# Kernel optimization log

Hardware: AMD Instinct MI355X
Metric: run time of the kernel (lower is better)

The kernel has to match this reference:

```python
import jax, jax.numpy as jnp
import numpy as np

NH = 16      # num_attention_heads
NKV = 8      # num_key_value_heads
G = NH // NKV  # num_key_value_groups
D = 128      # head_dim = hidden_size // NH
ROPE_MAX = 2048


def _rope_tables(seq_len, dtype=jnp.float32):
    # matches RotaryEmbedding: inv_freq over even dims, freqs duplicated (concat), cos/sin cached
    inv_freq = 1.0 / (10000.0 ** (jnp.arange(0, D, 2, dtype=jnp.float32) / D))
    t = jnp.arange(ROPE_MAX, dtype=jnp.float32)[:, None]          # [max, 1]
    freqs = t * inv_freq[None, :]                                  # [max, D/2]
    freqs = jnp.concatenate((freqs, freqs), axis=-1)               # [max, D]
    cos = jnp.cos(freqs)[:seq_len].astype(dtype)                   # [S, D]
    sin = jnp.sin(freqs)[:seq_len].astype(dtype)
    # unsqueeze(0) then unsqueeze(2) -> [1, S, 1, D] broadcasting over batch and heads
    return cos[None, :, None, :], sin[None, :, None, :]


def _rotate_half(x):
    x1, x2 = jnp.split(x, 2, axis=-1)
    return jnp.concatenate((-x2, x1), axis=-1)


def setup_inputs() -> dict:
    key = jax.random.key(0)
    ks = jax.random.split(key, 5)
    B, S, H = 2, 2048, 2048
    scale = 1.0 / np.sqrt(H)
    return {
        "hidden_states": jax.random.normal(ks[0], (B, S, H), jnp.float32),
        "Wq": jax.random.normal(ks[1], (H, H), jnp.float32) * scale,
        "Wk": jax.random.normal(ks[2], (NKV * D, H), jnp.float32) * scale,
        "Wv": jax.random.normal(ks[3], (NKV * D, H), jnp.float32) * scale,
        "Wo": jax.random.normal(ks[4], (H, H), jnp.float32) * scale,
    }


def reference(hidden_states, Wq, Wk, Wv, Wo):
    B, S, H = hidden_states.shape
    # projections (nn.Linear: y = x @ W.T, no bias)
    q = (hidden_states @ Wq.T).reshape(B, S, NH, D)     # [B,S,NH,D]
    k = (hidden_states @ Wk.T).reshape(B, S, NKV, D)    # [B,S,NKV,D]
    v = (hidden_states @ Wv.T).reshape(B, S, NKV, D)

    cos, sin = _rope_tables(S, hidden_states.dtype)
    q = q * cos + _rotate_half(q) * sin
    k = k * cos + _rotate_half(k) * sin

    # GQA: query head h attends to kv head h // G (repeat_kv ordering: h = n*G + g)
    qg = q.reshape(B, S, NKV, G, D).transpose(0, 2, 3, 1, 4)   # [B,NKV,G,S,D]
    kt = k.transpose(0, 2, 1, 3)                                # [B,NKV,S,D]
    vt = v.transpose(0, 2, 1, 3)                                # [B,NKV,S,D]

    scores = jnp.einsum("bngqd,bnkd->bngqk", qg, kt) / np.sqrt(D)  # [B,NKV,G,S,S]
    causal = jnp.triu(jnp.ones((S, S), dtype=bool), k=1)
    neg = jnp.finfo(scores.dtype).min
    scores = jnp.where(causal[None, None, None], neg, scores)
    probs = jax.nn.softmax(scores.astype(jnp.float32), axis=-1).astype(q.dtype)

    out = jnp.einsum("bngqk,bnkd->bngqd", probs, vt)            # [B,NKV,G,S,D]
    out = out.transpose(0, 3, 1, 2, 4).reshape(B, S, H)         # [B,S,H]
    return out @ Wo.T
```

## Files before the change

kernel.cpp:

```cpp
#include <hip/hip_runtime.h>

typedef unsigned short u16;
typedef __attribute__((ext_vector_type(8))) short short8;
typedef __attribute__((ext_vector_type(4))) float f32x4;

__device__ __forceinline__ u16 f2bf(float f) {
  unsigned u = __float_as_uint(f);
  return (u16)((u + 0x7FFFu + ((u >> 16) & 1u)) >> 16);
}
__device__ __forceinline__ float bf2f(u16 h) {
  return __uint_as_float(((unsigned)h) << 16);
}

__device__ __forceinline__ void gload_lds16(const void* g, void* l) {
  __builtin_amdgcn_global_load_lds(
      (const __attribute__((address_space(1))) unsigned*)g,
      (__attribute__((address_space(3))) unsigned*)l, 16, 0, 0);
}

__global__ void cast_f32_bf16_k(const float4* __restrict__ in, u16* __restrict__ out, int n4) {
  int i = blockIdx.x * 256 + threadIdx.x;
  if (i >= n4) return;
  float4 v = in[i];
  union { u16 u[4]; uint2 d; } r;
  r.u[0] = f2bf(v.x); r.u[1] = f2bf(v.y); r.u[2] = f2bf(v.z); r.u[3] = f2bf(v.w);
  *reinterpret_cast<uint2*>(out + (size_t)i * 4) = r.d;
}

__global__ void rope_tables_k(float* __restrict__ cosT, float* __restrict__ sinT) {
  int idx = blockIdx.x * 256 + threadIdx.x;
  int i = idx & 63, s = idx >> 6;
  double inv = pow(10000.0, -(double)(2 * i) / 128.0);
  double f = (double)s * inv;
  cosT[idx] = (float)cos(f);
  sinT[idx] = (float)sin(f);
}

__global__ void rope_q_k(u16* __restrict__ x, const float* __restrict__ cosT,
                         const float* __restrict__ sinT) {
  int idx = blockIdx.x * 256 + threadIdx.x;
  int i = idx & 63;
  int hh = (idx >> 6) & 15;
  int row = idx >> 10;
  int s = row & 2047;
  size_t base = (size_t)row * 4096 + hh * 128;
  float x1 = bf2f(x[base + i]);
  float x2 = bf2f(x[base + i + 64]);
  float c = cosT[s * 64 + i], sn = sinT[s * 64 + i];
  x[base + i]      = f2bf(x1 * c - x2 * sn);
  x[base + i + 64] = f2bf(x2 * c + x1 * sn);
}

__global__ void rope_repack_k_k(const u16* __restrict__ qkv, u16* __restrict__ kt,
                                const float* __restrict__ cosT, const float* __restrict__ sinT) {
  int idx = blockIdx.x * 256 + threadIdx.x;
  int i = idx & 63;
  int kvh = (idx >> 6) & 7;
  int row = idx >> 9;
  int s = row & 2047, b = row >> 11;
  size_t src = (size_t)row * 4096 + 2048 + kvh * 128;
  float x1 = bf2f(qkv[src + i]);
  float x2 = bf2f(qkv[src + i + 64]);
  float c = cosT[s * 64 + i], sn = sinT[s * 64 + i];
  size_t dst = ((size_t)(b * 8 + kvh) * 2048 + s) * 128;
  kt[dst + i]      = f2bf(x1 * c - x2 * sn);
  kt[dst + i + 64] = f2bf(x2 * c + x1 * sn);
}

__global__ void transpose_v_k(const u16* __restrict__ qkv, u16* __restrict__ vt) {
  __shared__ u16 tile[128][129];
  int bn = blockIdx.y;
  int s0 = blockIdx.x * 128;
  int b = bn >> 3, n = bn & 7;
  for (int e = threadIdx.x; e < 128 * 128; e += 256) {
    int r = e >> 7, c = e & 127;
    tile[r][c] = qkv[(size_t)(b * 2048 + s0 + r) * 4096 + 3072 + n * 128 + c];
  }
  __syncthreads();
  for (int e = threadIdx.x; e < 128 * 128; e += 256) {
    int r = e >> 7, c = e & 127;
    vt[((size_t)bn * 128 + r) * 2048 + s0 + c] = tile[c][r];
  }
}

template<typename OutT>
__global__ __launch_bounds__(256) void gemm_bt_k(
    const u16* __restrict__ A, const u16* __restrict__ Bm,
    OutT* __restrict__ C, int M, int N, int K)
{
  __shared__ __align__(16) u16 As[128 * 32];
  __shared__ __align__(16) u16 Bs[128 * 32];
  const int tid = threadIdx.x;
  const int wave = tid >> 6, lane = tid & 63;
  const int wr = wave >> 1, wc = wave & 1;
  const int lrow = lane & 15, lgrp = lane >> 4;
  const int nwg = (int)(gridDim.x * gridDim.y);
  const int f = (int)(blockIdx.y * gridDim.x + blockIdx.x);
  const int sw = (f & 7) * (nwg >> 3) + (f >> 3);
  const int bx = sw % gridDim.x, by = sw / gridDim.x;
  const int row0 = by * 128, col0 = bx * 128;

  f32x4 acc[4][4];
  #pragma unroll
  for (int m = 0; m < 4; ++m)
    #pragma unroll
    for (int n = 0; n < 4; ++n) acc[m][n] = (f32x4){0.f, 0.f, 0.f, 0.f};

  for (int k0 = 0; k0 < K; k0 += 32) {
    #pragma unroll
    for (int i = 0; i < 2; ++i) {
      int c = i * 256 + tid;
      int r = c >> 2, cc = ((c & 3) ^ (r & 3)) * 8;
      gload_lds16(A + (size_t)(row0 + r) * K + k0 + cc,
                  As + (size_t)(i * 256 + wave * 64) * 8);
      gload_lds16(Bm + (size_t)(col0 + r) * K + k0 + cc,
                  Bs + (size_t)(i * 256 + wave * 64) * 8);
    }
    __syncthreads();
    short8 af[4], bfr[4];
    #pragma unroll
    for (int m = 0; m < 4; ++m)
      af[m] = *reinterpret_cast<const short8*>(As + (wr * 64 + m * 16 + lrow) * 32 + (lgrp ^ (lrow & 3)) * 8);
    #pragma unroll
    for (int n = 0; n < 4; ++n)
      bfr[n] = *reinterpret_cast<const short8*>(Bs + (wc * 64 + n * 16 + lrow) * 32 + (lgrp ^ (lrow & 3)) * 8);
    #pragma unroll
    for (int m = 0; m < 4; ++m)
      #pragma unroll
      for (int n = 0; n < 4; ++n)
        acc[m][n] = __builtin_amdgcn_mfma_f32_16x16x32_bf16(af[m], bfr[n], acc[m][n], 0, 0, 0);
    __syncthreads();
  }
  #pragma unroll
  for (int m = 0; m < 4; ++m)
    #pragma unroll
    for (int n = 0; n < 4; ++n)
      #pragma unroll
      for (int j = 0; j < 4; ++j) {
        int r = row0 + wr * 64 + m * 16 + lgrp * 4 + j;
        int col = col0 + wc * 64 + n * 16 + lrow;
        float val = acc[m][n][j];
        if constexpr (sizeof(OutT) == 2) C[(size_t)r * N + col] = f2bf(val);
        else                             C[(size_t)r * N + col] = val;
      }
}

template<typename OutT>
__global__ __launch_bounds__(512, 1) void gemm256_k(
    const u16* __restrict__ A, const u16* __restrict__ Bm,
    OutT* __restrict__ C, int M, int N, int K)
{
  __shared__ __align__(16) u16 As[2][256 * 64];
  __shared__ __align__(16) u16 Bs[2][256 * 64];
  const int tid = threadIdx.x;
  const int wave = tid >> 6, lane = tid & 63;
  const int wm = wave >> 2, wn = wave & 3;
  const int lrow = lane & 15, lgrp = lane >> 4;
  const int gx = (int)gridDim.x;
  const int nwg = gx * (int)gridDim.y;
  const int f = (int)(blockIdx.y * gridDim.x + blockIdx.x);
  const int sw = (f & 7) * (nwg >> 3) + (f >> 3);
  const int bx = sw % gx, by = sw / gx;
  const int row0 = by * 256, col0 = bx * 256;

  f32x4 acc[8][4];
  #pragma unroll
  for (int m = 0; m < 8; ++m)
    #pragma unroll
    for (int n = 0; n < 4; ++n) acc[m][n] = (f32x4){0.f, 0.f, 0.f, 0.f};

  const int NT = K >> 6;

  auto stage = [&](int buf, int k0) {
    #pragma unroll
    for (int i = 0; i < 4; ++i) {
      int cid = i * 512 + tid;
      int row = cid >> 3, cp = cid & 7;
      int c = cp ^ (row & 7);
      gload_lds16(A + (size_t)(row0 + row) * K + k0 + c * 8,
                  &As[buf][(size_t)(i * 512 + wave * 64) * 8]);
      gload_lds16(Bm + (size_t)(col0 + row) * K + k0 + c * 8,
                  &Bs[buf][(size_t)(i * 512 + wave * 64) * 8]);
    }
  };

  stage(0, 0);
  for (int t = 0; t < NT; ++t) {
    const int cur = t & 1;
    if (t + 1 < NT) {
      stage(cur ^ 1, (t + 1) << 6);
      asm volatile("s_waitcnt vmcnt(8)" ::: "memory");
    } else {
      asm volatile("s_waitcnt vmcnt(0)" ::: "memory");
    }
    __builtin_amdgcn_s_barrier();
    __builtin_amdgcn_sched_barrier(0);
    #pragma unroll
    for (int ks = 0; ks < 2; ++ks) {
      short8 af[8], bfr[4];
      #pragma unroll
      for (int m = 0; m < 8; ++m) {
        int row = wm * 128 + m * 16 + lrow;
        int cp = (ks * 4 + lgrp) ^ (row & 7);
        af[m] = *reinterpret_cast<const short8*>(&As[cur][row * 64 + cp * 8]);
      }
      #pragma unroll
      for (int n = 0; n < 4; ++n) {
        int row = wn * 64 + n * 16 + lrow;
        int cp = (ks * 4 + lgrp) ^ (row & 7);
        bfr[n] = *reinterpret_cast<const short8*>(&Bs[cur][row * 64 + cp * 8]);
      }
      #pragma unroll
      for (int m = 0; m < 8; ++m)
        #pragma unroll
        for (int n = 0; n < 4; ++n)
          acc[m][n] = __builtin_amdgcn_mfma_f32_16x16x32_bf16(af[m], bfr[n], acc[m][n], 0, 0, 0);
    }
    __builtin_amdgcn_sched_barrier(0);
    __builtin_amdgcn_s_barrier();
  }

  #pragma unroll
  for (int m = 0; m < 8; ++m)
    #pragma unroll
    for (int n = 0; n < 4; ++n)
      #pragma unroll
      for (int j = 0; j < 4; ++j) {
        int r = row0 + wm * 128 + m * 16 + lgrp * 4 + j;
        int col = col0 + wn * 64 + n * 16 + lrow;
        float val = acc[m][n][j];
        if constexpr (sizeof(OutT) == 2) C[(size_t)r * N + col] = f2bf(val);
        else                             C[(size_t)r * N + col] = val;
      }
}

__global__ __launch_bounds__(256, 2) void flash_attn_k(
    const u16* __restrict__ qkv, const u16* __restrict__ kt,
    const u16* __restrict__ vt, u16* __restrict__ o)
{
  constexpr int S = 2048, NH = 16, NKV = 8, D = 128;
  const int wave = threadIdx.x >> 6, lane = threadIdx.x & 63;
  const int flat = blockIdx.x;
  const int pr = flat >> 5;
  const int bh = (flat & 7) * 4 + ((flat >> 3) & 3);
  const int b = bh >> 4, h = bh & 15;
  const int kvh = h >> 1;
  const int lrow = lane & 15, lgrp = lane >> 4;

  __shared__ __align__(16) u16 ks[2][64 * 128];
  __shared__ __align__(16) u16 vs[2][128 * 64];

  const float scl2 = 0.12754245006443634f;
  const u16* khead = kt + (size_t)(b * NKV + kvh) * S * D;
  const u16* vhead = vt + (size_t)(b * NKV + kvh) * D * S;

  auto stage = [&](int nxt, int kv0n) {
    #pragma unroll
    for (int i = 0; i < 4; ++i) {
      int c = i * 256 + wave * 64 + lane;
      int kr = c >> 4;
      int kc16 = (c & 15) ^ (kr & 7);
      gload_lds16(khead + (size_t)(kv0n + kr) * D + kc16 * 8,
                  &ks[nxt][(size_t)(i * 256 + wave * 64) * 8]);
      int vr = c >> 3;
      int vc = (c & 7) ^ (vr & 7);
      gload_lds16(vhead + (size_t)vr * S + kv0n + vc * 8,
                  &vs[nxt][(size_t)(i * 256 + wave * 64) * 8]);
    }
  };

  #pragma unroll
  for (int ph = 0; ph < 2; ++ph) {
    const int qt = ph ? pr : (31 - pr);
    const int q0 = qt * 64 + wave * 16;
    const int trips = qt + 1;

    short8 qf[4];
    const u16* qbase = qkv + (size_t)(b * S + q0 + lrow) * 4096 + h * 128;
    #pragma unroll
    for (int kc = 0; kc < 4; ++kc)
      qf[kc] = *reinterpret_cast<const short8*>(qbase + kc * 32 + lgrp * 8);

    f32x4 acc[8];
    #pragma unroll
    for (int n = 0; n < 8; ++n) acc[n] = (f32x4){0.f, 0.f, 0.f, 0.f};
    float l_part[4] = {0.f, 0.f, 0.f, 0.f};

    stage(0, 0);
    __syncthreads();

    for (int t = 0; t < trips; ++t) {
      const int cur = t & 1;
      const int kv0 = t * 64;
      f32x4 sc[4];
      #pragma unroll
      for (int nb = 0; nb < 4; ++nb) {
        sc[nb] = (f32x4){0.f, 0.f, 0.f, 0.f};
        const int r = nb * 16 + lrow;
        #pragma unroll
        for (int kc = 0; kc < 4; ++kc) {
          int ch = (kc * 4 + lgrp) ^ (r & 7);
          short8 kf = *reinterpret_cast<const short8*>(&ks[cur][r * 128 + ch * 8]);
          sc[nb] = __builtin_amdgcn_mfma_f32_16x16x32_bf16(qf[kc], kf, sc[nb], 0, 0, 0);
        }
      }
      __syncthreads();
      if (t + 1 < trips) stage(cur ^ 1, kv0 + 64);
      u16* pb = &ks[cur][wave * 1024];
      if (t < trips - 1) {
        #pragma unroll
        for (int nb = 0; nb < 4; ++nb)
          #pragma unroll
          for (int j = 0; j < 4; ++j) {
            int qr = lgrp * 4 + j;
            float p = exp2f(fminf(sc[nb][j] * scl2, 43.f));
            l_part[j] += p;
            pb[qr * 64 + ((nb * 16 + lrow) ^ ((qr & 7) << 3))] = f2bf(p);
          }
      } else {
        #pragma unroll
        for (int nb = 0; nb < 4; ++nb) {
          if (nb < wave) {
            #pragma unroll
            for (int j = 0; j < 4; ++j) {
              int qr = lgrp * 4 + j;
              float p = exp2f(fminf(sc[nb][j] * scl2, 43.f));
              l_part[j] += p;
              pb[qr * 64 + ((nb * 16 + lrow) ^ ((qr & 7) << 3))] = f2bf(p);
            }
          } else if (nb == wave) {
            #pragma unroll
            for (int j = 0; j < 4; ++j) {
              int qr = lgrp * 4 + j;
              float p = (lrow <= qr) ? exp2f(fminf(sc[nb][j] * scl2, 43.f)) : 0.f;
              l_part[j] += p;
              pb[qr * 64 + ((nb * 16 + lrow) ^ ((qr & 7) << 3))] = f2bf(p);
            }
          } else {
            #pragma unroll
            for (int j = 0; j < 4; ++j) {
              int qr = lgrp * 4 + j;
              pb[qr * 64 + ((nb * 16 + lrow) ^ ((qr & 7) << 3))] = 0;
            }
          }
        }
      }
      short8 pf[2];
      #pragma unroll
      for (int kc2 = 0; kc2 < 2; ++kc2) {
        int ch = (kc2 * 4 + lgrp) ^ (lrow & 7);
        pf[kc2] = *reinterpret_cast<const short8*>(&pb[lrow * 64 + ch * 8]);
      }
      #pragma unroll
      for (int n = 0; n < 8; ++n) {
        const int d = n * 16 + lrow;
        #pragma unroll
        for (int kc2 = 0; kc2 < 2; ++kc2) {
          int ch = (kc2 * 4 + lgrp) ^ (d & 7);
          short8 vf = *reinterpret_cast<const short8*>(&vs[cur][d * 64 + ch * 8]);
          acc[n] = __builtin_amdgcn_mfma_f32_16x16x32_bf16(pf[kc2], vf, acc[n], 0, 0, 0);
        }
      }
      __syncthreads();
    }

    float inv[4];
    #pragma unroll
    for (int j = 0; j < 4; ++j) {
      float s = l_part[j];
      #pragma unroll
      for (int off = 8; off; off >>= 1) s += __shfl_xor(s, off);
      inv[j] = 1.f / s;
    }
    u16* obase = o + (((size_t)(b * S + q0)) * NH + h) * D;
    #pragma unroll
    for (int n = 0; n < 8; ++n)
      #pragma unroll
      for (int j = 0; j < 4; ++j)
        obase[(size_t)(lgrp * 4 + j) * NH * D + n * 16 + lrow] = f2bf(acc[n][j] * inv[j]);
    __syncthreads();
  }
}

extern "C" void kernel_launch(void* const* d_in, const int* in_sizes, int n_in,
                              void* d_out, int out_size, void* d_ws, size_t ws_size,
                              hipStream_t stream) {
  const float* hs = (const float*)d_in[0];
  const float* Wq = (const float*)d_in[1];
  const float* Wk = (const float*)d_in[2];
  const float* Wv = (const float*)d_in[3];
  const float* Wo = (const float*)d_in[4];
  float* out = (float*)d_out;

  constexpr int B = 2, S = 2048, H = 2048, NH = 16, NKV = 8, D = 128;
  constexpr int M = B * S;
  constexpr int NQKV = 4096;

  char* w = (char*)d_ws;
  auto alloc = [&](size_t bytes) { char* p = w; w += (bytes + 255) & ~(size_t)255; return p; };
  u16* hs_bf   = (u16*)alloc((size_t)M * H * 2);
  u16* wqkv_bf = (u16*)alloc((size_t)NQKV * H * 2);
  u16* wo_bf   = (u16*)alloc((size_t)H * H * 2);
  u16* qkv     = (u16*)alloc((size_t)M * NQKV * 2);
  float* cosT  = (float*)alloc((size_t)S * 64 * 4);
  float* sinT  = (float*)alloc((size_t)S * 64 * 4);
  u16* attn = hs_bf;
  u16* vt   = wqkv_bf;
  u16* kt   = wqkv_bf + (size_t)B * NKV * D * S;

  cast_f32_bf16_k<<<(M * H / 4) / 256, 256, 0, stream>>>((const float4*)hs, hs_bf, M * H / 4);
  cast_f32_bf16_k<<<(H * H / 4) / 256, 256, 0, stream>>>((const float4*)Wq, wqkv_bf, H * H / 4);
  cast_f32_bf16_k<<<(NKV * D * H / 4) / 256, 256, 0, stream>>>((const float4*)Wk, wqkv_bf + (size_t)2048 * H, NKV * D * H / 4);
  cast_f32_bf16_k<<<(NKV * D * H / 4) / 256, 256, 0, stream>>>((const float4*)Wv, wqkv_bf + (size_t)3072 * H, NKV * D * H / 4);
  cast_f32_bf16_k<<<(H * H / 4) / 256, 256, 0, stream>>>((const float4*)Wo, wo_bf, H * H / 4);
  rope_tables_k<<<(S * 64) / 256, 256, 0, stream>>>(cosT, sinT);

  gemm256_k<u16><<<dim3(NQKV / 256, M / 256), 512, 0, stream>>>(hs_bf, wqkv_bf, qkv, M, NQKV, H);

  rope_q_k<<<(M * 16 * 64) / 256, 256, 0, stream>>>(qkv, cosT, sinT);
  rope_repack_k_k<<<(M * 8 * 64) / 256, 256, 0, stream>>>(qkv, kt, cosT, sinT);
  transpose_v_k<<<dim3(S / 128, B * NKV), 256, 0, stream>>>(qkv, vt);

  flash_attn_k<<<512, 256, 0, stream>>>(qkv, kt, vt, attn);

  gemm_bt_k<float><<<dim3(H / 128, M / 128), 256, 0, stream>>>(attn, wo_bf, out, M, H, H);
}
```

Before: 242.0 us.

## Deepen GEMM pipeline to four K=32 stages and switch LDS swizzle to rotation

The 256x256 GEMM kernel now works in K chunks of 32 instead of 64 and keeps four LDS buffers in flight, issuing three stages ahead with matching vmcnt waits. This hides more global-load latency at the same LDS footprint. Both GEMM kernels also replace the XOR swizzle with a rotation-based placement, (p + row/4) mod 4, intended to avoid LDS bank conflicts on the short8 fragment reads. The trade-off is twice as many barriers per K and less MFMA work between them.

```diff
diff --git a/kernel.cpp b/kernel.cpp
--- a/kernel.cpp
+++ b/kernel.cpp
@@ -106,24 +106,27 @@
     #pragma unroll
     for (int n = 0; n < 4; ++n) acc[m][n] = (f32x4){0.f, 0.f, 0.f, 0.f};
 
+  const int prd = (lgrp - (lrow >> 2)) & 3;
+
   for (int k0 = 0; k0 < K; k0 += 32) {
     #pragma unroll
     for (int i = 0; i < 2; ++i) {
       int c = i * 256 + tid;
-      int r = c >> 2, cc = ((c & 3) ^ (r & 3)) * 8;
-      gload_lds16(A + (size_t)(row0 + r) * K + k0 + cc,
+      int r = c >> 2, p = c & 3;
+      int g = (p + (r >> 2)) & 3;
+      gload_lds16(A + (size_t)(row0 + r) * K + k0 + g * 8,
                   As + (size_t)(i * 256 + wave * 64) * 8);
-      gload_lds16(Bm + (size_t)(col0 + r) * K + k0 + cc,
+      gload_lds16(Bm + (size_t)(col0 + r) * K + k0 + g * 8,
                   Bs + (size_t)(i * 256 + wave * 64) * 8);
     }
     __syncthreads();
     short8 af[4], bfr[4];
     #pragma unroll
     for (int m = 0; m < 4; ++m)
-      af[m] = *reinterpret_cast<const short8*>(As + (wr * 64 + m * 16 + lrow) * 32 + (lgrp ^ (lrow & 3)) * 8);
+      af[m] = *reinterpret_cast<const short8*>(As + (wr * 64 + m * 16 + lrow) * 32 + prd * 8);
     #pragma unroll
     for (int n = 0; n < 4; ++n)
-      bfr[n] = *reinterpret_cast<const short8*>(Bs + (wc * 64 + n * 16 + lrow) * 32 + (lgrp ^ (lrow & 3)) * 8);
+      bfr[n] = *reinterpret_cast<const short8*>(Bs + (wc * 64 + n * 16 + lrow) * 32 + prd * 8);
     #pragma unroll
     for (int m = 0; m < 4; ++m)
       #pragma unroll
@@ -150,8 +153,8 @@
     const u16* __restrict__ A, const u16* __restrict__ Bm,
     OutT* __restrict__ C, int M, int N, int K)
 {
-  __shared__ __align__(16) u16 As[2][256 * 64];
-  __shared__ __align__(16) u16 Bs[2][256 * 64];
+  __shared__ __align__(16) u16 As[4][256 * 32];
+  __shared__ __align__(16) u16 Bs[4][256 * 32];
   const int tid = threadIdx.x;
   const int wave = tid >> 6, lane = tid & 63;
   const int wm = wave >> 2, wn = wave & 3;
@@ -169,53 +172,54 @@
     #pragma unroll
     for (int n = 0; n < 4; ++n) acc[m][n] = (f32x4){0.f, 0.f, 0.f, 0.f};
 
-  const int NT = K >> 6;
-
-  auto stage = [&](int buf, int k0) {
-    #pragma unroll
-    for (int i = 0; i < 4; ++i) {
+  const int NT = K >> 5;
+  const int prd = (lgrp - (lrow >> 2)) & 3;
+
+  auto stage = [&](int buf, int t) {
+    const int k0 = t << 5;
+    #pragma unroll
+    for (int i = 0; i < 2; ++i) {
       int cid = i * 512 + tid;
-      int row = cid >> 3, cp = cid & 7;
-      int c = cp ^ (row & 7);
-      gload_lds16(A + (size_t)(row0 + row) * K + k0 + c * 8,
+      int row = cid >> 2, p = cid & 3;
+      int g = (p + (row >> 2)) & 3;
+      gload_lds16(A + (size_t)(row0 + row) * K + k0 + g * 8,
                   &As[buf][(size_t)(i * 512 + wave * 64) * 8]);
-      gload_lds16(Bm + (size_t)(col0 + row) * K + k0 + c * 8,
+      gload_lds16(Bm + (size_t)(col0 + row) * K + k0 + g * 8,
                   &Bs[buf][(size_t)(i * 512 + wave * 64) * 8]);
     }
   };
 
-  stage(0, 0);
+  stage(0, 0); stage(1, 1); stage(2, 2);
   for (int t = 0; t < NT; ++t) {
-    const int cur = t & 1;
-    if (t + 1 < NT) {
-      stage(cur ^ 1, (t + 1) << 6);
+    const int cur = t & 3;
+    if (t + 3 < NT) {
+      stage((t + 3) & 3, t + 3);
+      asm volatile("s_waitcnt vmcnt(12)" ::: "memory");
+    } else if (t + 3 == NT) {
       asm volatile("s_waitcnt vmcnt(8)" ::: "memory");
+    } else if (t + 2 == NT) {
+      asm volatile("s_waitcnt vmcnt(4)" ::: "memory");
     } else {
       asm volatile("s_waitcnt vmcnt(0)" ::: "memory");
     }
     __builtin_amdgcn_s_barrier();
     __builtin_amdgcn_sched_barrier(0);
-    #pragma unroll
-    for (int ks = 0; ks < 2; ++ks) {
-      short8 af[8], bfr[4];
-      #pragma unroll
-      for (int m = 0; m < 8; ++m) {
-        int row = wm * 128 + m * 16 + lrow;
-        int cp = (ks * 4 + lgrp) ^ (row & 7);
-        af[m] = *reinterpret_cast<const short8*>(&As[cur][row * 64 + cp * 8]);
-      }
-      #pragma unroll
-      for (int n = 0; n < 4; ++n) {
-        int row = wn * 64 + n * 16 + lrow;
-        int cp = (ks * 4 + lgrp) ^ (row & 7);
-        bfr[n] = *reinterpret_cast<const short8*>(&Bs[cur][row * 64 + cp * 8]);
-      }
-      #pragma unroll
-      for (int m = 0; m < 8; ++m)
-        #pragma unroll
-        for (int n = 0; n < 4; ++n)
-          acc[m][n] = __builtin_amdgcn_mfma_f32_16x16x32_bf16(af[m], bfr[n], acc[m][n], 0, 0, 0);
-    }
+    short8 af[8], bfr[4];
+    #pragma unroll
+    for (int m = 0; m < 8; ++m) {
+      int row = wm * 128 + m * 16 + lrow;
+      af[m] = *reinterpret_cast<const short8*>(&As[cur][row * 32 + prd * 8]);
+    }
+    #pragma unroll
+    for (int n = 0; n < 4; ++n) {
+      int row = wn * 64 + n * 16 + lrow;
+      bfr[n] = *reinterpret_cast<const short8*>(&Bs[cur][row * 32 + prd * 8]);
+    }
+    #pragma unroll
+    for (int m = 0; m < 8; ++m)
+      #pragma unroll
+      for (int n = 0; n < 4; ++n)
+        acc[m][n] = __builtin_amdgcn_mfma_f32_16x16x32_bf16(af[m], bfr[n], acc[m][n], 0, 0, 0);
     __builtin_amdgcn_sched_barrier(0);
     __builtin_amdgcn_s_barrier();
   }
```

Result: slower. 258.4 us (+6.8%).
